# Kernel tuning notes

Hardware: AMD Instinct MI355X
Metric: run time of the kernel (lower is better)

The kernel has to match this reference:

```python
import jax, jax.numpy as jnp
import jax.scipy as jsp
import numpy as np

H, W, C = 2048, 2048, 3
SCALE, TRANSLATE, ROTATE, SHEAR = 1.15, 0.15, np.pi / 12, 0.0


def _rotation_matrix(r):
    rx, ry = jnp.cos(r), jnp.sin(r)
    return jnp.array([[rx, ry, 0.0], [-ry, rx, 0.0], [0.0, 0.0, 1.0]])


def _scale_matrix(s):
    return jnp.array([[s, 0.0, 0.0], [0.0, s, 0.0], [0.0, 0.0, 1.0]])


def _shear_matrix(r):
    sh = jnp.tan(r)
    return jnp.array([[1.0, sh, 0.0], [0.0, 1.0, 0.0], [0.0, 0.0, 1.0]])


def _translation_matrix(tx, ty):
    return jnp.array([[1.0, 0.0, tx], [0.0, 1.0, ty], [0.0, 0.0, 1.0]])


def setup_inputs() -> dict:
    key = jax.random.key(0)
    k_img, k1, k2, k3, k4, k5 = jax.random.split(key, 6)
    image = jax.random.normal(k_img, (H, W, C), dtype=jnp.float32)
    # Random affine params exactly as RandomAffine.__call__ samples them.
    scale = jax.random.uniform(k1, minval=1.0, maxval=SCALE)
    tx = jax.random.uniform(k2, minval=-TRANSLATE, maxval=TRANSLATE) * W
    ty = jax.random.uniform(k3, minval=-TRANSLATE, maxval=TRANSLATE) * H
    rotation = jax.random.uniform(k4, minval=-1.0, maxval=1.0) * ROTATE
    shear = jax.random.uniform(k5, minval=-1.0, maxval=1.0) * SHEAR
    matrix = (_rotation_matrix(rotation) @ _scale_matrix(scale)
              @ _shear_matrix(shear) @ _translation_matrix(tx, ty))
    return {"image": image, "matrix": matrix.astype(jnp.float32)}


def _apply_affine(image, matrix):
    h, w, c = image.shape
    dtype = image.dtype
    y = jnp.linspace(-h / 2, h / 2, num=h)
    x = jnp.linspace(-w / 2, w / 2, num=w)
    v = jnp.ones(1)
    ch = jnp.arange(3)
    # (h, w, 1, 3, 4) grid of homogeneous coords [y, x, 1, channel]
    coords = jnp.stack(jnp.meshgrid(y, x, v, ch, indexing='ij'), axis=-1).astype(dtype)
    transform = jnp.eye(4, dtype=dtype).at[:-1, :-1].set(matrix.astype(dtype))
    coords = coords @ transform + jnp.array([h / 2, w / 2, 0.0, 0.0], dtype=dtype)
    # drop the homogeneous slot (index -2), keep (y, x, channel)
    coords = jnp.concatenate([coords[..., :2], coords[..., 3:]], axis=-1)
    # 'h w v c yxc -> yxc (h w v c)'
    coords = coords.reshape(-1, 3).T  # (3, h*w*3)
    out = jsp.ndimage.map_coordinates(
        image, [coords[0], coords[1], coords[2]], order=1, mode='reflect')
    return out.reshape(h, w, c)


def reference(image, matrix):
    return _apply_affine(image, matrix)
```

## Files before the change

kernel.cpp:

```cpp
#include <hip/hip_runtime.h>


#define IMG_H 2048
#define IMG_W 2048

__device__ __forceinline__ int reflect2048(int i) {
    int p = i & 4095;
    return (p < 2048) ? p : (4095 - p);
}

__global__ __launch_bounds__(256) void affine_reflect_kernel(
    const float* __restrict__ img, const float* __restrict__ M,
    float* __restrict__ out)
{
    int idx = blockIdx.x * 256 + threadIdx.x;
    int i = idx >> 11;
    int j = idx & 2047;

    const float step = 2048.0f / 2047.0f;
    float yv = fmaf((float)i, step, -1024.0f);
    float xv = fmaf((float)j, step, -1024.0f);

    float m00 = M[0], m01 = M[1];
    float m10 = M[3], m11 = M[4];
    float m20 = M[6], m21 = M[7];

    float ry = yv * m00 + xv * m10 + (m20 + 1024.0f);
    float rx = yv * m01 + xv * m11 + (m21 + 1024.0f);

    float fy = floorf(ry), fx = floorf(rx);
    float wy1 = ry - fy, wx1 = rx - fx;
    float wy0 = 1.0f - wy1, wx0 = 1.0f - wx1;

    int iy = (int)fy, ix = (int)fx;
    int iy0 = reflect2048(iy),     iy1 = reflect2048(iy + 1);
    int ix0 = reflect2048(ix),     ix1 = reflect2048(ix + 1);

    const float* r0 = img + iy0 * (IMG_W * 3);
    const float* r1 = img + iy1 * (IMG_W * 3);
    int c0 = ix0 * 3, c1 = ix1 * 3;

    float w00 = wy0 * wx0, w01 = wy0 * wx1;
    float w10 = wy1 * wx0, w11 = wy1 * wx1;

    int o = idx * 3;
    #pragma unroll
    for (int c = 0; c < 3; ++c) {
        float v = w00 * r0[c0 + c] + w01 * r0[c1 + c]
                + w10 * r1[c0 + c] + w11 * r1[c1 + c];
        out[o + c] = v;
    }
}

extern "C" void kernel_launch(void* const* d_in, const int* in_sizes, int n_in,
                              void* d_out, int out_size, void* d_ws, size_t ws_size,
                              hipStream_t stream) {
    const float* img = (const float*)d_in[0];
    const float* M   = (const float*)d_in[1];
    float* out = (float*)d_out;

    dim3 grid((IMG_H * IMG_W) / 256), block(256);
    hipLaunchKernelGGL(affine_reflect_kernel, grid, block, 0, stream, img, M, out);
}
```

Measured before the change: 109.1 us.

## Stage per-tile source bounding box in LDS for bilinear affine sampling

Each block now handles a 32x32 output tile. It first computes the transformed corners to get the source bounding box, cooperatively loads a 52x52x3 reflected patch into shared memory, then does the bilinear interpolation from LDS. This replaces scattered global gathers with mostly contiguous row loads and reuse within the tile. In exchange it loads a larger patch than it strictly needs, and the 32KB of LDS per block lowers occupancy. Correctness relies on the rotation and scale ranges keeping the footprint inside 52 pixels.

```diff
diff --git a/kernel.cpp b/kernel.cpp
--- a/kernel.cpp
+++ b/kernel.cpp
@@ -3,52 +3,88 @@
 
 #define IMG_H 2048
 #define IMG_W 2048
+#define TILE  32
+#define BBH   52
+#define BBW   52
+#define BBW3  (BBW * 3)
+#define BBN   (BBH * BBW3)
 
 __device__ __forceinline__ int reflect2048(int i) {
     int p = i & 4095;
     return (p < 2048) ? p : (4095 - p);
 }
 
-__global__ __launch_bounds__(256) void affine_reflect_kernel(
-    const float* __restrict__ img, const float* __restrict__ M,
+__global__ __launch_bounds__(256) void affine_tile_kernel(
+    const float* __restrict__ img, const float* __restrict__ Mp,
     float* __restrict__ out)
 {
-    int idx = blockIdx.x * 256 + threadIdx.x;
-    int i = idx >> 11;
-    int j = idx & 2047;
+    __shared__ float lds[BBN];
+
+    const int tid = threadIdx.x;
+    const int tbx = blockIdx.x & 63;
+    const int tby = blockIdx.x >> 6;
+    const int i0 = tby * TILE, j0 = tbx * TILE;
 
     const float step = 2048.0f / 2047.0f;
-    float yv = fmaf((float)i, step, -1024.0f);
-    float xv = fmaf((float)j, step, -1024.0f);
+    const float m00 = Mp[0], m01 = Mp[1];
+    const float m10 = Mp[3], m11 = Mp[4];
+    const float b0 = Mp[6] + 1024.0f, b1 = Mp[7] + 1024.0f;
 
-    float m00 = M[0], m01 = M[1];
-    float m10 = M[3], m11 = M[4];
-    float m20 = M[6], m21 = M[7];
+    const float yv0 = fmaf((float)i0,            step, -1024.0f);
+    const float yv1 = fmaf((float)(i0 + TILE-1), step, -1024.0f);
+    const float xv0 = fmaf((float)j0,            step, -1024.0f);
+    const float xv1 = fmaf((float)(j0 + TILE-1), step, -1024.0f);
 
-    float ry = yv * m00 + xv * m10 + (m20 + 1024.0f);
-    float rx = yv * m01 + xv * m11 + (m21 + 1024.0f);
+    const float rya = yv0*m00 + xv0*m10 + b0, ryb = yv0*m00 + xv1*m10 + b0;
+    const float ryc = yv1*m00 + xv0*m10 + b0, ryd = yv1*m00 + xv1*m10 + b0;
+    const float rxa = yv0*m01 + xv0*m11 + b1, rxb = yv0*m01 + xv1*m11 + b1;
+    const float rxc = yv1*m01 + xv0*m11 + b1, rxd = yv1*m01 + xv1*m11 + b1;
 
-    float fy = floorf(ry), fx = floorf(rx);
-    float wy1 = ry - fy, wx1 = rx - fx;
-    float wy0 = 1.0f - wy1, wx0 = 1.0f - wx1;
+    const float min_ry = fminf(fminf(rya, ryb), fminf(ryc, ryd));
+    const float min_rx = fminf(fminf(rxa, rxb), fminf(rxc, rxd));
 
-    int iy = (int)fy, ix = (int)fx;
-    int iy0 = reflect2048(iy),     iy1 = reflect2048(iy + 1);
-    int ix0 = reflect2048(ix),     ix1 = reflect2048(ix + 1);
+    const int y0 = (int)floorf(min_ry) - 1;
+    const int x0 = (int)floorf(min_rx) - 1;
 
-    const float* r0 = img + iy0 * (IMG_W * 3);
-    const float* r1 = img + iy1 * (IMG_W * 3);
-    int c0 = ix0 * 3, c1 = ix1 * 3;
+    for (int e = tid; e < BBN; e += 256) {
+        int byy = e / BBW3;
+        int k   = e - byy * BBW3;
+        int xx  = k / 3;
+        int ch  = k - xx * 3;
+        int gy  = reflect2048(y0 + byy);
+        int gx  = reflect2048(x0 + xx);
+        lds[e] = img[(gy * IMG_W + gx) * 3 + ch];
+    }
+    __syncthreads();
 
-    float w00 = wy0 * wx0, w01 = wy0 * wx1;
-    float w10 = wy1 * wx0, w11 = wy1 * wx1;
+    #pragma unroll
+    for (int r = 0; r < 4; ++r) {
+        const int li = r * 8 + (tid >> 5);
+        const int lj = tid & 31;
+        const int i = i0 + li, j = j0 + lj;
 
-    int o = idx * 3;
-    #pragma unroll
-    for (int c = 0; c < 3; ++c) {
-        float v = w00 * r0[c0 + c] + w01 * r0[c1 + c]
-                + w10 * r1[c0 + c] + w11 * r1[c1 + c];
-        out[o + c] = v;
+        const float yv = fmaf((float)i, step, -1024.0f);
+        const float xv = fmaf((float)j, step, -1024.0f);
+        const float ry = yv*m00 + xv*m10 + b0;
+        const float rx = yv*m01 + xv*m11 + b1;
+
+        const float fy = floorf(ry), fx = floorf(rx);
+        const float wy1 = ry - fy, wx1 = rx - fx;
+        const float wy0 = 1.0f - wy1, wx0 = 1.0f - wx1;
+
+        const int iy = (int)fy - y0;
+        const int ix = (int)fx - x0;
+
+        const float* p0 = &lds[iy * BBW3 + ix * 3];
+        const float* p1 = p0 + BBW3;
+
+        const float w00 = wy0*wx0, w01 = wy0*wx1;
+        const float w10 = wy1*wx0, w11 = wy1*wx1;
+
+        const int o = (i * IMG_W + j) * 3;
+        out[o + 0] = w00*p0[0] + w01*p0[3] + w10*p1[0] + w11*p1[3];
+        out[o + 1] = w00*p0[1] + w01*p0[4] + w10*p1[1] + w11*p1[4];
+        out[o + 2] = w00*p0[2] + w01*p0[5] + w10*p1[2] + w11*p1[5];
     }
 }
 
@@ -59,6 +95,6 @@
     const float* M   = (const float*)d_in[1];
     float* out = (float*)d_out;
 
-    dim3 grid((IMG_H * IMG_W) / 256), block(256);
-    hipLaunchKernelGGL(affine_reflect_kernel, grid, block, 0, stream, img, M, out);
+    dim3 grid((IMG_H / TILE) * (IMG_W / TILE)), block(256);
+    hipLaunchKernelGGL(affine_tile_kernel, grid, block, 0, stream, img, M, out);
 }
```

Measured after the change: 120.4 us. 1.1x slower.
